# Kernel tuning notes

Measured on AMD Instinct MI355X. Metric: run time of the kernel, lower is better.

The kernel has to match this reference:

```python
import jax, jax.numpy as jnp
import numpy as np

N, E, F, S = 20000, 160000, 16, 8
ECC1, ECC2, ECC3 = 40, 24, 24
DS = [96, 256, 768, 512, 64, 1]


def setup_inputs() -> dict:
    key = jax.random.key(0)
    ks = iter(jax.random.split(key, 40))
    inp = {}
    inp["x"] = jax.random.normal(next(ks), (N, F), dtype=jnp.float32)
    inp["edge_index"] = jax.random.randint(next(ks), (E, 2), 0, N, dtype=jnp.int32)
    inp["e"] = jax.random.uniform(next(ks), (E, S), dtype=jnp.float32)

    def dense_p(k, fi, fo):
        return (jax.random.normal(k, (fi, fo), dtype=jnp.float32) * (1.0 / np.sqrt(fi)),
                jnp.zeros((fo,), dtype=jnp.float32))

    # ECCConv params: kernel_network dense (S -> F_in*F_out), root kernel, bias
    for i, (fi, fo) in enumerate([(F, ECC1), (ECC1, ECC2), (ECC2, ECC3)], start=1):
        We, be = dense_p(next(ks), S, fi * fo)
        root, _ = dense_p(next(ks), fi, fo)
        inp[f"We{i}"], inp[f"be{i}"] = We, be
        inp[f"root{i}"], inp[f"b{i}"] = root, jnp.zeros((fo,), dtype=jnp.float32)

    dims = [ECC3] + DS
    for i in range(6):
        W, b = dense_p(next(ks), dims[i], dims[i + 1])
        inp[f"Wd{i+1}"], inp[f"bd{i+1}"] = W, b
    return inp


def _ecc(h, src, tgt, e, We, be, root, b):
    fi, fo = root.shape
    # per-edge filter matrices from edge features: [E, F_in, F_out]
    K = (e @ We + be).reshape(e.shape[0], fi, fo)
    msg = jnp.einsum('ef,efo->eo', h[src], K)          # gather + per-edge matvec
    agg = jax.ops.segment_sum(msg, tgt, num_segments=h.shape[0])  # scatter-add
    return jax.nn.relu(agg + h @ root + b)


def reference(x, edge_index, e,
              We1, be1, root1, b1,
              We2, be2, root2, b2,
              We3, be3, root3, b3,
              Wd1, bd1, Wd2, bd2, Wd3, bd3, Wd4, bd4, Wd5, bd5, Wd6, bd6):
    src, tgt = edge_index[:, 0], edge_index[:, 1]
    h = _ecc(x, src, tgt, e, We1, be1, root1, b1)
    h = _ecc(h, src, tgt, e, We2, be2, root2, b2)
    h = _ecc(h, src, tgt, e, We3, be3, root3, b3)
    g = jnp.sum(h, axis=0, keepdims=True)  # GlobalSumPool (single mode) -> [1, 24]
    for W, b in [(Wd1, bd1), (Wd2, bd2), (Wd3, bd3), (Wd4, bd4), (Wd5, bd5)]:
        g = jax.nn.relu(g @ W + b)
    return g @ Wd6 + bd6  # [1, 1]
```

## Files before the change

### kernel.cpp

```cpp
#include <hip/hip_runtime.h>

constexpr int NN  = 20000;
constexpr int NE  = 160000;
constexpr int CAP = 32;
constexpr int TN  = 32;
constexpr int NBM = 16;

__device__ inline void gstore(float* p, float v) {
    __hip_atomic_store(p, v, __ATOMIC_RELAXED, __HIP_MEMORY_SCOPE_AGENT);
}
__device__ inline float gload(const float* p) {
    return __hip_atomic_load(p, __ATOMIC_RELAXED, __HIP_MEMORY_SCOPE_AGENT);
}

__device__ inline void mbarrier(int* ctr, int target, bool wait) {
    __syncthreads();
    if (threadIdx.x == 0) {
        __threadfence();
        __hip_atomic_fetch_add(ctr, 1, __ATOMIC_ACQ_REL, __HIP_MEMORY_SCOPE_AGENT);
        if (wait)
            while (__hip_atomic_load(ctr, __ATOMIC_ACQUIRE, __HIP_MEMORY_SCOPE_AGENT) < target) {}
    }
    __syncthreads();
}

template<int FI, int FO2>
__device__ void stage_W(float* Wlds, const float* __restrict__ We,
                        const float* __restrict__ be, const float* __restrict__ root)
{
    constexpr int PW = 10 * FO2, C4 = PW / 4, O4 = FO2 / 4;
    for (int t = threadIdx.x; t < FI * C4; t += 256) {
        const int f = t / C4, r = t % C4, s = r / O4, oq = r % O4;
        const float4* src;
        if (s < 8)       src = (const float4*)(We + (size_t)s * FI * FO2 + f * FO2 + oq * 4);
        else if (s == 8) src = (const float4*)(be + f * FO2 + oq * 4);
        else             src = (const float4*)(root + f * FO2 + oq * 4);
        ((float4*)Wlds)[t] = *src;
    }
}

template<int FI, int FO2>
__device__ void gemm_tile(const float* htile, const float* Wlds,
                          const float* __restrict__ bias, float* __restrict__ Pout, int n0)
{
    constexpr int PW = 10 * FO2, C4 = PW / 4, O4 = FO2 / 4;
    constexpr int TPN = 256 / TN;
    const int nl = threadIdx.x / TPN;
    const int lane = threadIdx.x % TPN;
    const int n = n0 + nl;
    if (n >= NN) return;
    const float*  hr = &htile[nl * (FI + 4)];
    const float4* W4 = (const float4*)Wlds;
    float4* Pr = (float4*)(Pout + (size_t)n * PW);
    for (int cc = lane; cc < C4; cc += TPN) {
        float4 a = {0.f, 0.f, 0.f, 0.f};
        #pragma unroll
        for (int f = 0; f < FI; f++) {
            const float  hf = hr[f];
            const float4 w  = W4[f * C4 + cc];
            a.x = fmaf(hf, w.x, a.x); a.y = fmaf(hf, w.y, a.y);
            a.z = fmaf(hf, w.z, a.z); a.w = fmaf(hf, w.w, a.w);
        }
        if (cc >= 9 * O4) {
            const float4 b4 = ((const float4*)bias)[cc - 9 * O4];
            a.x += b4.x; a.y += b4.y; a.z += b4.z; a.w += b4.w;
        }
        Pr[cc] = a;
    }
}

__global__ __launch_bounds__(256)
void fill_nodeP1_kernel(const int* __restrict__ eidx, const float* __restrict__ e,
                        const float* __restrict__ x,
                        const float* __restrict__ We1, const float* __restrict__ be1,
                        const float* __restrict__ root1, const float* __restrict__ b1,
                        int* __restrict__ cnt, int* __restrict__ adjsrc,
                        float* __restrict__ esort, float* __restrict__ Pa)
{
    __shared__ float smem[16 * 400 + TN * 20];
    const int b = blockIdx.x, tid = threadIdx.x;
    if (b < 625) {
        const int eid = b * 256 + tid;
        const int2 st = ((const int2*)eidx)[eid];
        const int q = atomicAdd(&cnt[st.y], 1);
        if (q < CAP) {
            const int slot = st.y * CAP + q;
            adjsrc[slot] = st.x;
            const float4* e4 = (const float4*)(e + (size_t)eid * 8);
            float4* o4 = (float4*)(esort + (size_t)slot * 8);
            o4[0] = e4[0];
            o4[1] = e4[1];
        }
    } else {
        float* Wlds  = smem;
        float* htile = smem + 6400;
        stage_W<16, 40>(Wlds, We1, be1, root1);
        const int n0 = (b - 625) * TN;
        for (int t = tid; t < TN * 4; t += 256) {
            const int nl = t / 4, fq = t % 4;
            const int n = n0 + nl;
            float4 v = {0.f, 0.f, 0.f, 0.f};
            if (n < NN) v = ((const float4*)(x + (size_t)n * 16))[fq];
            *((float4*)&htile[nl * 20 + fq * 4]) = v;
        }
        __syncthreads();
        gemm_tile<16, 40>(htile, Wlds, b1, Pa, n0);
    }
}

template<int FO, int FO2>
__global__ __launch_bounds__(256)
void gather_nodeP_kernel(const float* __restrict__ Pin, const int* __restrict__ cnt,
                         const int* __restrict__ adjsrc, const float* __restrict__ esort,
                         const float* __restrict__ We2, const float* __restrict__ be2,
                         const float* __restrict__ root2, const float* __restrict__ b2,
                         float* __restrict__ Pout)
{
    constexpr int PW1 = 10 * FO;
    constexpr int WSZ = FO * 10 * FO2;
    __shared__ float smem[WSZ + TN * (FO + 4)];
    float* Wlds  = smem;
    float* htile = smem + WSZ;
    stage_W<FO, FO2>(Wlds, We2, be2, root2);

    const int n0 = blockIdx.x * TN;
    for (int T = threadIdx.x; T < TN * FO; T += 256) {
        const int nl = T / FO, o = T % FO;
        const int n = n0 + nl;
        float acc = 0.f;
        if (n < NN) {
            acc = Pin[(size_t)n * PW1 + 9 * FO + o];
            const int d = min(cnt[n], CAP);
            const int*   ab    = adjsrc + n * CAP;
            const float* ebase = esort + (size_t)n * CAP * 8;
            #pragma unroll 2
            for (int j = 0; j < d; j++) {
                const int src = ab[j];
                const float* Pr = Pin + (size_t)src * PW1 + o;
                const float* eq = ebase + j * 8;
                float a = Pr[8 * FO];
                #pragma unroll
                for (int s = 0; s < 8; s++)
                    a = fmaf(eq[s], Pr[s * FO], a);
                acc += a;
            }
        }
        htile[nl * (FO + 4) + o] = fmaxf(acc, 0.f);
    }
    __syncthreads();
    gemm_tile<FO, FO2>(htile, Wlds, b2, Pout, n0);
}

__global__ __launch_bounds__(256)
void gather_colsum_kernel(const float* __restrict__ Pin, const int* __restrict__ cnt,
                          const int* __restrict__ adjsrc, const float* __restrict__ esort,
                          float* __restrict__ g)
{
    constexpr int FO = 24, PW1 = 240;
    __shared__ float gl[FO];
    const int tid = threadIdx.x;
    if (tid < FO) gl[tid] = 0.f;
    __syncthreads();

    const int n0 = blockIdx.x * TN;
    for (int T = tid; T < TN * FO; T += 256) {
        const int nl = T / FO, o = T % FO;
        const int n = n0 + nl;
        if (n >= NN) continue;
        float acc = Pin[(size_t)n * PW1 + 9 * FO + o];
        const int d = min(cnt[n], CAP);
        const int*   ab    = adjsrc + n * CAP;
        const float* ebase = esort + (size_t)n * CAP * 8;
        #pragma unroll 2
        for (int j = 0; j < d; j++) {
            const int src = ab[j];
            const float* Pr = Pin + (size_t)src * PW1 + o;
            const float* eq = ebase + j * 8;
            float a = Pr[8 * FO];
            #pragma unroll
            for (int s = 0; s < 8; s++)
                a = fmaf(eq[s], Pr[s * FO], a);
            acc += a;
        }
        atomicAdd(&gl[o], fmaxf(acc, 0.f));
    }
    __syncthreads();
    if (tid < FO) unsafeAtomicAdd(&g[tid], gl[tid]);
}

__global__ __launch_bounds__(256)
void mlp_kernel(const float* __restrict__ g, int* __restrict__ ctr,
                const float* __restrict__ Wd1, const float* __restrict__ bd1,
                const float* __restrict__ Wd2, const float* __restrict__ bd2,
                const float* __restrict__ Wd3, const float* __restrict__ bd3,
                const float* __restrict__ Wd4, const float* __restrict__ bd4,
                const float* __restrict__ Wd5, const float* __restrict__ bd5,
                const float* __restrict__ Wd6, const float* __restrict__ bd6,
                float* __restrict__ m1, float* __restrict__ m2,
                float* __restrict__ m3, float* __restrict__ m4,
                float* __restrict__ m5, float* __restrict__ out)
{
    __shared__ float xs[768];
    __shared__ float red[256];
    const int tid = threadIdx.x, b = blockIdx.x;

    if (tid < 24) xs[tid] = g[tid];
    __syncthreads();
    if (tid < 6) {
        const int o = b * 6 + tid;
        float a = bd1[o];
        #pragma unroll
        for (int i = 0; i < 24; i++) a = fmaf(xs[i], Wd1[i * 96 + o], a);
        gstore(&m1[o], fmaxf(a, 0.f));
    }
    mbarrier(ctr, 1 * NBM, true);

    if (tid < 96) xs[tid] = gload(&m1[tid]);
    __syncthreads();
    {
        const int o = (tid & 15), kg = tid >> 4;
        float a = 0.f;
        #pragma unroll
        for (int i = kg * 6; i < kg * 6 + 6; i++)
            a = fmaf(xs[i], Wd2[i * 256 + b * 16 + o], a);
        red[tid] = a;
    }
    __syncthreads();
    if (tid < 16) {
        float s = bd2[b * 16 + tid];
        #pragma unroll
        for (int k = 0; k < 16; k++) s += red[k * 16 + tid];
        gstore(&m2[b * 16 + tid], fmaxf(s, 0.f));
    }
    mbarrier(ctr, 2 * NBM, true);

    for (int i = tid; i < 256; i += 256) xs[i] = gload(&m2[i]);
    __syncthreads();
    if (tid < 192) {
        const int o = b * 48 + (tid % 48), kg = tid / 48;
        float a = 0.f;
        #pragma unroll 8
        for (int i = kg * 64; i < kg * 64 + 64; i++)
            a = fmaf(xs[i], Wd3[(size_t)i * 768 + o], a);
        red[tid] = a;
    }
    __syncthreads();
    if (tid < 48) {
        float s = bd3[b * 48 + tid] + red[tid] + red[48 + tid] + red[96 + tid] + red[144 + tid];
        gstore(&m3[b * 48 + tid], fmaxf(s, 0.f));
    }
    mbarrier(ctr, 3 * NBM, true);

    for (int i = tid; i < 768; i += 256) xs[i] = gload(&m3[i]);
    __syncthreads();
    {
        const int o = b * 32 + (tid & 31), kg = tid >> 5;
        float a = 0.f;
        #pragma unroll 8
        for (int i = kg * 96; i < kg * 96 + 96; i++)
            a = fmaf(xs[i], Wd4[(size_t)i * 512 + o], a);
        red[tid] = a;
    }
    __syncthreads();
    if (tid < 32) {
        float s = bd4[b * 32 + tid];
        #pragma unroll
        for (int k = 0; k < 8; k++) s += red[k * 32 + tid];
        gstore(&m4[b * 32 + tid], fmaxf(s, 0.f));
    }
    mbarrier(ctr, 4 * NBM, true);

    for (int i = tid; i < 512; i += 256) xs[i] = gload(&m4[i]);
    __syncthreads();
    {
        const int o = (tid & 3), kg = tid >> 2;
        float a = 0.f;
        #pragma unroll
        for (int i = kg * 8; i < kg * 8 + 8; i++)
            a = fmaf(xs[i], Wd5[(size_t)i * 64 + b * 4 + o], a);
        red[tid] = a;
    }
    __syncthreads();
    if (tid < 4) {
        float s = bd5[b * 4 + tid];
        #pragma unroll
        for (int k = 0; k < 64; k++) s += red[k * 4 + tid];
        gstore(&m5[b * 4 + tid], fmaxf(s, 0.f));
    }
    mbarrier(ctr, 5 * NBM, b == 0);

    if (b == 0 && tid < 64) {
        float v = gload(&m5[tid]) * Wd6[tid];
        #pragma unroll
        for (int off = 32; off > 0; off >>= 1)
            v += __shfl_down(v, off, 64);
        if (tid == 0) out[0] = v + bd6[0];
    }
}

extern "C" void kernel_launch(void* const* d_in, const int* in_sizes, int n_in,
                              void* d_out, int out_size, void* d_ws, size_t ws_size,
                              hipStream_t stream)
{
    const float* x     = (const float*)d_in[0];
    const int*   eidx  = (const int*)  d_in[1];
    const float* e     = (const float*)d_in[2];
    const float* We1   = (const float*)d_in[3];  const float* be1 = (const float*)d_in[4];
    const float* root1 = (const float*)d_in[5];  const float* b1  = (const float*)d_in[6];
    const float* We2   = (const float*)d_in[7];  const float* be2 = (const float*)d_in[8];
    const float* root2 = (const float*)d_in[9];  const float* b2  = (const float*)d_in[10];
    const float* We3   = (const float*)d_in[11]; const float* be3 = (const float*)d_in[12];
    const float* root3 = (const float*)d_in[13]; const float* b3  = (const float*)d_in[14];
    const float* Wd1 = (const float*)d_in[15]; const float* bd1 = (const float*)d_in[16];
    const float* Wd2 = (const float*)d_in[17]; const float* bd2 = (const float*)d_in[18];
    const float* Wd3 = (const float*)d_in[19]; const float* bd3 = (const float*)d_in[20];
    const float* Wd4 = (const float*)d_in[21]; const float* bd4 = (const float*)d_in[22];
    const float* Wd5 = (const float*)d_in[23]; const float* bd5 = (const float*)d_in[24];
    const float* Wd6 = (const float*)d_in[25]; const float* bd6 = (const float*)d_in[26];

    int*   wi     = (int*)d_ws;
    int*   cnt    = wi;
    float* g      = (float*)d_ws + 20000;
    int*   mctr   = wi + 20032;
    float* m1     = (float*)d_ws + 20064;
    float* m2     = m1 + 96;
    float* m3     = m2 + 256;
    float* m4     = m3 + 768;
    float* m5     = m4 + 512;
    int*   adjsrc = wi + 21760;
    float* wf     = (float*)d_ws;
    float* esort  = wf + 661760;
    float* Pa     = wf + 5781760;
    float* Pb     = wf + 13781760;

    hipMemsetAsync(d_ws, 0, (size_t)21760 * sizeof(int), stream);

    fill_nodeP1_kernel<<<1250, 256, 0, stream>>>(eidx, e, x, We1, be1, root1, b1,
                                                 cnt, adjsrc, esort, Pa);

    gather_nodeP_kernel<40, 24><<<625, 256, 0, stream>>>(Pa, cnt, adjsrc, esort,
                                                         We2, be2, root2, b2, Pb);

    gather_nodeP_kernel<24, 24><<<625, 256, 0, stream>>>(Pb, cnt, adjsrc, esort,
                                                         We3, be3, root3, b3, Pa);

    gather_colsum_kernel<<<625, 256, 0, stream>>>(Pa, cnt, adjsrc, esort, g);

    mlp_kernel<<<NBM, 256, 0, stream>>>(g, mctr,
                                        Wd1, bd1, Wd2, bd2, Wd3, bd3,
                                        Wd4, bd4, Wd5, bd5, Wd6, bd6,
                                        m1, m2, m3, m4, m5, (float*)d_out);
}
```

Measured before the change: 270.2 us.

## Switch edge aggregation from gather-by-target to push-by-source message slots

Builds a source-sorted adjacency in which each edge records its destination slot in a target-major message buffer. Each layer kernel computes a node's transform, then pushes per-edge messages (8-way edge-weighted combination of its own P row) into the slots owned by the target. The next layer reduces those slots contiguously instead of doing random gathers of P rows. The weight staging is also split into two halves so that LDS use shrinks. The trade is an extra large message buffer written and reread through global memory, a second atomic counter per edge, and scattered message writes.

```diff
diff --git a/kernel.cpp b/kernel.cpp
--- a/kernel.cpp
+++ b/kernel.cpp
@@ -12,7 +12,6 @@
 __device__ inline float gload(const float* p) {
     return __hip_atomic_load(p, __ATOMIC_RELAXED, __HIP_MEMORY_SCOPE_AGENT);
 }
-
 __device__ inline void mbarrier(int* ctr, int target, bool wait) {
     __syncthreads();
     if (threadIdx.x == 0) {
@@ -24,139 +23,142 @@
     __syncthreads();
 }
 
-template<int FI, int FO2>
-__device__ void stage_W(float* Wlds, const float* __restrict__ We,
-                        const float* __restrict__ be, const float* __restrict__ root)
-{
-    constexpr int PW = 10 * FO2, C4 = PW / 4, O4 = FO2 / 4;
-    for (int t = threadIdx.x; t < FI * C4; t += 256) {
-        const int f = t / C4, r = t % C4, s = r / O4, oq = r % O4;
-        const float4* src;
-        if (s < 8)       src = (const float4*)(We + (size_t)s * FI * FO2 + f * FO2 + oq * 4);
-        else if (s == 8) src = (const float4*)(be + f * FO2 + oq * 4);
-        else             src = (const float4*)(root + f * FO2 + oq * 4);
-        ((float4*)Wlds)[t] = *src;
-    }
-}
-
-template<int FI, int FO2>
-__device__ void gemm_tile(const float* htile, const float* Wlds,
-                          const float* __restrict__ bias, float* __restrict__ Pout, int n0)
-{
-    constexpr int PW = 10 * FO2, C4 = PW / 4, O4 = FO2 / 4;
-    constexpr int TPN = 256 / TN;
-    const int nl = threadIdx.x / TPN;
-    const int lane = threadIdx.x % TPN;
+__global__ __launch_bounds__(256)
+void fill_kernel(const int* __restrict__ eidx, const float* __restrict__ e,
+                 int* __restrict__ cnt_t, int* __restrict__ cnt_s,
+                 int* __restrict__ adj_t, float* __restrict__ e_src)
+{
+    const int eid = blockIdx.x * 256 + threadIdx.x;
+    const int2 st = ((const int2*)eidx)[eid];
+    const int qt = atomicAdd(&cnt_t[st.y], 1);
+    const int qs = atomicAdd(&cnt_s[st.x], 1);
+    if (qs < CAP) {
+        const size_t ss = (size_t)st.x * CAP + qs;
+        adj_t[ss] = (qt < CAP) ? st.y * CAP + qt : -1;
+        const float4* e4 = (const float4*)(e + (size_t)eid * 8);
+        float4* o4 = (float4*)(e_src + ss * 8);
+        o4[0] = e4[0];
+        o4[1] = e4[1];
+    }
+}
+
+template<int FI, int FO2, bool FIRST>
+__global__ __launch_bounds__(256)
+void layer_kernel(const float* __restrict__ x,
+                  const float* __restrict__ Pprev,
+                  const float* __restrict__ msgin,
+                  const int* __restrict__ cnt_t, const int* __restrict__ cnt_s,
+                  const int* __restrict__ adj_t, const float* __restrict__ e_src,
+                  const float* __restrict__ We, const float* __restrict__ be,
+                  const float* __restrict__ root, const float* __restrict__ bias,
+                  float* __restrict__ Pout,
+                  float* __restrict__ msgout)
+{
+    constexpr int PW  = 10 * FO2;
+    constexpr int C4  = PW / 4;
+    constexpr int C4H = C4 / 2;
+    constexpr int O4  = FO2 / 4;
+    constexpr int PWP = 10 * FI;
+    constexpr int HS  = FI + 4;
+
+    __shared__ float Wlds[FI * C4H * 4];
+    __shared__ float htile[TN * HS];
+    const int tid = threadIdx.x;
+    const int n0 = blockIdx.x * TN;
+
+    if (FIRST) {
+        for (int t = tid; t < TN * (FI / 4); t += 256) {
+            const int nl = t / (FI / 4), fq = t % (FI / 4);
+            ((float4*)&htile[nl * HS])[fq] =
+                ((const float4*)(x + (size_t)(n0 + nl) * FI))[fq];
+        }
+    } else {
+        for (int T = tid; T < TN * FI; T += 256) {
+            const int nl = T / FI, o = T % FI;
+            const int n = n0 + nl;
+            float acc = Pprev[(size_t)n * PWP + 9 * FI + o];
+            const int d = min(cnt_t[n], CAP);
+            const float* mb = msgin + (size_t)n * CAP * FI + o;
+            #pragma unroll 4
+            for (int j = 0; j < d; j++) acc += mb[(size_t)j * FI];
+            htile[nl * HS + o] = fmaxf(acc, 0.f);
+        }
+    }
+
+    const int nl = tid >> 3, lane = tid & 7;
     const int n = n0 + nl;
-    if (n >= NN) return;
-    const float*  hr = &htile[nl * (FI + 4)];
-    const float4* W4 = (const float4*)Wlds;
-    float4* Pr = (float4*)(Pout + (size_t)n * PW);
-    for (int cc = lane; cc < C4; cc += TPN) {
-        float4 a = {0.f, 0.f, 0.f, 0.f};
-        #pragma unroll
-        for (int f = 0; f < FI; f++) {
-            const float  hf = hr[f];
-            const float4 w  = W4[f * C4 + cc];
-            a.x = fmaf(hf, w.x, a.x); a.y = fmaf(hf, w.y, a.y);
-            a.z = fmaf(hf, w.z, a.z); a.w = fmaf(hf, w.w, a.w);
-        }
-        if (cc >= 9 * O4) {
-            const float4 b4 = ((const float4*)bias)[cc - 9 * O4];
-            a.x += b4.x; a.y += b4.y; a.z += b4.z; a.w += b4.w;
-        }
-        Pr[cc] = a;
+    const float* hr = &htile[nl * HS];
+    float4* Pr4 = (float4*)(Pout + (size_t)n * PW);
+    #pragma unroll
+    for (int half = 0; half < 2; half++) {
+        __syncthreads();
+        for (int t = tid; t < FI * C4H; t += 256) {
+            const int f = t / C4H, cq = t % C4H;
+            const int cc = half * C4H + cq;
+            const int s = cc / O4, oq = cc % O4;
+            const float* src;
+            if (s < 8)       src = We + (size_t)s * FI * FO2 + f * FO2 + oq * 4;
+            else if (s == 8) src = be + f * FO2 + oq * 4;
+            else             src = root + f * FO2 + oq * 4;
+            ((float4*)Wlds)[t] = *(const float4*)src;
+        }
+        __syncthreads();
+        const float4* W4 = (const float4*)Wlds;
+        for (int cq = lane; cq < C4H; cq += 8) {
+            const int cc = half * C4H + cq;
+            float4 a = {0.f, 0.f, 0.f, 0.f};
+            #pragma unroll
+            for (int f = 0; f < FI; f++) {
+                const float  hf = hr[f];
+                const float4 w  = W4[f * C4H + cq];
+                a.x = fmaf(hf, w.x, a.x); a.y = fmaf(hf, w.y, a.y);
+                a.z = fmaf(hf, w.z, a.z); a.w = fmaf(hf, w.w, a.w);
+            }
+            if (cc >= 9 * O4) {
+                const float4 b4 = ((const float4*)bias)[cc - 9 * O4];
+                a.x += b4.x; a.y += b4.y; a.z += b4.z; a.w += b4.w;
+            }
+            Pr4[cc] = a;
+        }
+    }
+    __syncthreads();
+
+    const int ds = min(cnt_s[n], CAP);
+    const float4* Pr = (const float4*)(Pout + (size_t)n * PW);
+    for (int j = lane; j < ds; j += 8) {
+        const size_t ss = (size_t)n * CAP + j;
+        const int st = adj_t[ss];
+        if (st < 0) continue;
+        const float4* e4 = (const float4*)(e_src + ss * 8);
+        const float4 ea = e4[0], eb = e4[1];
+        const float es[8] = {ea.x, ea.y, ea.z, ea.w, eb.x, eb.y, eb.z, eb.w};
+        float4 acc[O4];
+        #pragma unroll
+        for (int q = 0; q < O4; q++) acc[q] = Pr[8 * O4 + q];
+        #pragma unroll
+        for (int s = 0; s < 8; s++) {
+            const float w = es[s];
+            #pragma unroll
+            for (int q = 0; q < O4; q++) {
+                const float4 v = Pr[s * O4 + q];
+                acc[q].x = fmaf(w, v.x, acc[q].x);
+                acc[q].y = fmaf(w, v.y, acc[q].y);
+                acc[q].z = fmaf(w, v.z, acc[q].z);
+                acc[q].w = fmaf(w, v.w, acc[q].w);
+            }
+        }
+        float4* mo = (float4*)(msgout + (size_t)st * FO2);
+        #pragma unroll
+        for (int q = 0; q < O4; q++) mo[q] = acc[q];
     }
 }
 
 __global__ __launch_bounds__(256)
-void fill_nodeP1_kernel(const int* __restrict__ eidx, const float* __restrict__ e,
-                        const float* __restrict__ x,
-                        const float* __restrict__ We1, const float* __restrict__ be1,
-                        const float* __restrict__ root1, const float* __restrict__ b1,
-                        int* __restrict__ cnt, int* __restrict__ adjsrc,
-                        float* __restrict__ esort, float* __restrict__ Pa)
-{
-    __shared__ float smem[16 * 400 + TN * 20];
-    const int b = blockIdx.x, tid = threadIdx.x;
-    if (b < 625) {
-        const int eid = b * 256 + tid;
-        const int2 st = ((const int2*)eidx)[eid];
-        const int q = atomicAdd(&cnt[st.y], 1);
-        if (q < CAP) {
-            const int slot = st.y * CAP + q;
-            adjsrc[slot] = st.x;
-            const float4* e4 = (const float4*)(e + (size_t)eid * 8);
-            float4* o4 = (float4*)(esort + (size_t)slot * 8);
-            o4[0] = e4[0];
-            o4[1] = e4[1];
-        }
-    } else {
-        float* Wlds  = smem;
-        float* htile = smem + 6400;
-        stage_W<16, 40>(Wlds, We1, be1, root1);
-        const int n0 = (b - 625) * TN;
-        for (int t = tid; t < TN * 4; t += 256) {
-            const int nl = t / 4, fq = t % 4;
-            const int n = n0 + nl;
-            float4 v = {0.f, 0.f, 0.f, 0.f};
-            if (n < NN) v = ((const float4*)(x + (size_t)n * 16))[fq];
-            *((float4*)&htile[nl * 20 + fq * 4]) = v;
-        }
-        __syncthreads();
-        gemm_tile<16, 40>(htile, Wlds, b1, Pa, n0);
-    }
-}
-
-template<int FO, int FO2>
-__global__ __launch_bounds__(256)
-void gather_nodeP_kernel(const float* __restrict__ Pin, const int* __restrict__ cnt,
-                         const int* __restrict__ adjsrc, const float* __restrict__ esort,
-                         const float* __restrict__ We2, const float* __restrict__ be2,
-                         const float* __restrict__ root2, const float* __restrict__ b2,
-                         float* __restrict__ Pout)
-{
-    constexpr int PW1 = 10 * FO;
-    constexpr int WSZ = FO * 10 * FO2;
-    __shared__ float smem[WSZ + TN * (FO + 4)];
-    float* Wlds  = smem;
-    float* htile = smem + WSZ;
-    stage_W<FO, FO2>(Wlds, We2, be2, root2);
-
-    const int n0 = blockIdx.x * TN;
-    for (int T = threadIdx.x; T < TN * FO; T += 256) {
-        const int nl = T / FO, o = T % FO;
-        const int n = n0 + nl;
-        float acc = 0.f;
-        if (n < NN) {
-            acc = Pin[(size_t)n * PW1 + 9 * FO + o];
-            const int d = min(cnt[n], CAP);
-            const int*   ab    = adjsrc + n * CAP;
-            const float* ebase = esort + (size_t)n * CAP * 8;
-            #pragma unroll 2
-            for (int j = 0; j < d; j++) {
-                const int src = ab[j];
-                const float* Pr = Pin + (size_t)src * PW1 + o;
-                const float* eq = ebase + j * 8;
-                float a = Pr[8 * FO];
-                #pragma unroll
-                for (int s = 0; s < 8; s++)
-                    a = fmaf(eq[s], Pr[s * FO], a);
-                acc += a;
-            }
-        }
-        htile[nl * (FO + 4) + o] = fmaxf(acc, 0.f);
-    }
-    __syncthreads();
-    gemm_tile<FO, FO2>(htile, Wlds, b2, Pout, n0);
-}
-
-__global__ __launch_bounds__(256)
-void gather_colsum_kernel(const float* __restrict__ Pin, const int* __restrict__ cnt,
-                          const int* __restrict__ adjsrc, const float* __restrict__ esort,
-                          float* __restrict__ g)
-{
-    constexpr int FO = 24, PW1 = 240;
+void gather_colsum_kernel(const float* __restrict__ P3,
+                          const float* __restrict__ msg3,
+                          const int* __restrict__ cnt_t, float* __restrict__ g)
+{
+    constexpr int FO = 24;
     __shared__ float gl[FO];
     const int tid = threadIdx.x;
     if (tid < FO) gl[tid] = 0.f;
@@ -166,22 +168,11 @@
     for (int T = tid; T < TN * FO; T += 256) {
         const int nl = T / FO, o = T % FO;
         const int n = n0 + nl;
-        if (n >= NN) continue;
-        float acc = Pin[(size_t)n * PW1 + 9 * FO + o];
-        const int d = min(cnt[n], CAP);
-        const int*   ab    = adjsrc + n * CAP;
-        const float* ebase = esort + (size_t)n * CAP * 8;
-        #pragma unroll 2
-        for (int j = 0; j < d; j++) {
-            const int src = ab[j];
-            const float* Pr = Pin + (size_t)src * PW1 + o;
-            const float* eq = ebase + j * 8;
-            float a = Pr[8 * FO];
-            #pragma unroll
-            for (int s = 0; s < 8; s++)
-                a = fmaf(eq[s], Pr[s * FO], a);
-            acc += a;
-        }
+        float acc = P3[(size_t)n * 240 + 9 * FO + o];
+        const int d = min(cnt_t[n], CAP);
+        const float* mb = msg3 + (size_t)n * CAP * FO + o;
+        #pragma unroll 4
+        for (int j = 0; j < d; j++) acc += mb[(size_t)j * FO];
         atomicAdd(&gl[o], fmaxf(acc, 0.f));
     }
     __syncthreads();
@@ -318,33 +309,42 @@
     const float* Wd5 = (const float*)d_in[23]; const float* bd5 = (const float*)d_in[24];
     const float* Wd6 = (const float*)d_in[25]; const float* bd6 = (const float*)d_in[26];
 
-    int*   wi     = (int*)d_ws;
-    int*   cnt    = wi;
-    float* g      = (float*)d_ws + 20000;
-    int*   mctr   = wi + 20032;
-    float* m1     = (float*)d_ws + 20064;
-    float* m2     = m1 + 96;
-    float* m3     = m2 + 256;
-    float* m4     = m3 + 768;
-    float* m5     = m4 + 512;
-    int*   adjsrc = wi + 21760;
-    float* wf     = (float*)d_ws;
-    float* esort  = wf + 661760;
-    float* Pa     = wf + 5781760;
-    float* Pb     = wf + 13781760;
-
-    hipMemsetAsync(d_ws, 0, (size_t)21760 * sizeof(int), stream);
-
-    fill_nodeP1_kernel<<<1250, 256, 0, stream>>>(eidx, e, x, We1, be1, root1, b1,
-                                                 cnt, adjsrc, esort, Pa);
-
-    gather_nodeP_kernel<40, 24><<<625, 256, 0, stream>>>(Pa, cnt, adjsrc, esort,
-                                                         We2, be2, root2, b2, Pb);
-
-    gather_nodeP_kernel<24, 24><<<625, 256, 0, stream>>>(Pb, cnt, adjsrc, esort,
-                                                         We3, be3, root3, b3, Pa);
-
-    gather_colsum_kernel<<<625, 256, 0, stream>>>(Pa, cnt, adjsrc, esort, g);
+    int*   wi    = (int*)d_ws;
+    int*   cnt_t = wi;
+    int*   cnt_s = wi + 20000;
+    float* g     = (float*)d_ws + 40000;
+    int*   mctr  = wi + 40032;
+    float* m1    = (float*)d_ws + 40064;
+    float* m2    = m1 + 96;
+    float* m3    = m2 + 256;
+    float* m4    = m3 + 768;
+    float* m5    = m4 + 512;
+    int*   adj_t = wi + 41760;
+    float* wf    = (float*)d_ws;
+    float* e_src = wf + 681760;
+    float* msgA  = wf + 5801760;
+    float* msgB  = wf + 31401760;
+    float* Pa    = wf + 46761760;
+    float* Pb    = wf + 54761760;
+    float* Pc    = wf + 59561760;
+
+    hipMemsetAsync(d_ws, 0, (size_t)41760 * sizeof(int), stream);
+
+    fill_kernel<<<625, 256, 0, stream>>>(eidx, e, cnt_t, cnt_s, adj_t, e_src);
+
+    layer_kernel<16, 40, true><<<625, 256, 0, stream>>>(
+        x, nullptr, nullptr, cnt_t, cnt_s, adj_t, e_src,
+        We1, be1, root1, b1, Pa, msgA);
+
+    layer_kernel<40, 24, false><<<625, 256, 0, stream>>>(
+        nullptr, Pa, msgA, cnt_t, cnt_s, adj_t, e_src,
+        We2, be2, root2, b2, Pb, msgB);
+
+    layer_kernel<24, 24, false><<<625, 256, 0, stream>>>(
+        nullptr, Pb, msgB, cnt_t, cnt_s, adj_t, e_src,
+        We3, be3, root3, b3, Pc, msgA);
+
+    gather_colsum_kernel<<<625, 256, 0, stream>>>(Pc, msgA, cnt_t, g);
 
     mlp_kernel<<<NBM, 256, 0, stream>>>(g, mctr,
                                         Wd1, bd1, Wd2, bd2, Wd3, bd3,
```

New measurement: 277.4 us. 1.03x slower.
